# Optimization experiments

Hardware: AMD Instinct MI355X
Metric: run time of the kernel (lower is better)

## Reference

```python
import jax, jax.numpy as jnp
import numpy as np

B, S, HID = 2, 2048, 2048
H, HKV, D = 16, 8, 128
CHUNK = 512
THETA = 1000000.0
NEG = -1e9


def setup_inputs() -> dict:
    key = jax.random.key(0)
    ks = jax.random.split(key, 10)
    hidden_states = jax.random.normal(ks[0], (B, S, HID), dtype=jnp.float32)
    # additive causal mask (0 on/below diagonal, -1e9 above)
    tri = jnp.tril(jnp.ones((S, S), dtype=bool))
    attention_mask = jnp.where(tri, 0.0, NEG).astype(jnp.float32)
    attention_mask = jnp.broadcast_to(attention_mask[None, None], (B, 1, S, S))
    w = 0.02
    Wq = jax.random.normal(ks[1], (HID, H * D), dtype=jnp.float32) * w
    bq = jax.random.normal(ks[2], (H * D,), dtype=jnp.float32) * w
    Wk = jax.random.normal(ks[3], (HID, HKV * D), dtype=jnp.float32) * w
    bk = jax.random.normal(ks[4], (HKV * D,), dtype=jnp.float32) * w
    Wv = jax.random.normal(ks[5], (HID, HKV * D), dtype=jnp.float32) * w
    bv = jax.random.normal(ks[6], (HKV * D,), dtype=jnp.float32) * w
    Wo = jax.random.normal(ks[7], (H * D, HID), dtype=jnp.float32) * w
    bo = jax.random.normal(ks[8], (HID,), dtype=jnp.float32) * w
    return {"hidden_states": hidden_states, "attention_mask": attention_mask,
            "Wq": Wq, "bq": bq, "Wk": Wk, "bk": bk, "Wv": Wv, "bv": bv,
            "Wo": Wo, "bo": bo}


def _rope_tables(seq_len, dim):
    inv_freq = 1.0 / (THETA ** (jnp.arange(0, dim, 2, dtype=jnp.float32) / dim))
    pos = jnp.arange(seq_len, dtype=jnp.float32)
    freqs = pos[:, None] * inv_freq[None, :]          # [S, D/2]
    emb = jnp.concatenate([freqs, freqs], axis=-1)    # [S, D]
    return jnp.cos(emb)[None, None], jnp.sin(emb)[None, None]  # [1,1,S,D]


def _rotate_half(x):
    x1, x2 = jnp.split(x, 2, axis=-1)
    return jnp.concatenate([-x2, x1], axis=-1)


def _attn_forward(hidden_states, attention_mask, Wq, bq, Wk, bk, Wv, bv, Wo, bo):
    bsz, s, _ = hidden_states.shape
    q = (hidden_states @ Wq + bq).reshape(bsz, s, H, D).transpose(0, 2, 1, 3)
    k = (hidden_states @ Wk + bk).reshape(bsz, s, HKV, D).transpose(0, 2, 1, 3)
    v = (hidden_states @ Wv + bv).reshape(bsz, s, HKV, D).transpose(0, 2, 1, 3)
    cos, sin = _rope_tables(s, D)
    q = q * cos + _rotate_half(q) * sin
    k = k * cos + _rotate_half(k) * sin
    n_rep = H // HKV
    k = jnp.repeat(k, n_rep, axis=1)  # repeat_kv
    v = jnp.repeat(v, n_rep, axis=1)
    scale = 1.0 / jnp.sqrt(jnp.float32(D))
    nq, nk = s // CHUNK, s // CHUNK
    Qc = q.reshape(bsz, H, nq, CHUNK, D)
    Kc = jnp.moveaxis(k.reshape(bsz, H, nk, CHUNK, D), 2, 0)   # [nk,B,H,Ck,D]
    Vc = jnp.moveaxis(v.reshape(bsz, H, nk, CHUNK, D), 2, 0)
    Mc = jnp.moveaxis(attention_mask.reshape(bsz, 1, nq, CHUNK, nk, CHUNK), 4, 0)  # [nk,B,1,nq,Cq,Ck]

    def step(carry, xs):
        o, m, d = carry
        k_seg, v_seg, m_seg = xs
        # scores: [B,H,nq,Cq,Ck]
        sc = jnp.einsum('bhqcd,bhkd->bhqck', Qc, k_seg) * scale + m_seg
        new_m = jnp.maximum(m, sc.max(axis=-1, keepdims=True))
        e = jnp.exp(sc - new_m)
        sums = e.sum(axis=-1, keepdims=True)
        prev = jnp.exp(m - new_m)          # NOTE: uses running max, as in source
        d_new = prev + sums
        o = (o * prev + jnp.einsum('bhqck,bhkd->bhqcd', e, v_seg)) / d_new
        return (o, new_m, d_new), None

    o0 = jnp.zeros((bsz, H, nq, CHUNK, D), dtype=jnp.float32)
    m0 = jnp.full((bsz, H, nq, CHUNK, 1), -jnp.inf, dtype=jnp.float32)
    d0 = jnp.ones((bsz, H, nq, CHUNK, 1), dtype=jnp.float32)
    (o, m, d), _ = jax.lax.scan(step, (o0, m0, d0), (Kc, Vc, Mc))
    # final rescale: attn_output * exp(max - logsumexp) == o / d_last (source math)
    o = o / d
    attn = o.reshape(bsz, H, s, D).transpose(0, 2, 1, 3).reshape(bsz, s, H * D)
    return attn @ Wo + bo


def reference(hidden_states, attention_mask, Wq, bq, Wk, bk, Wv, bv, Wo, bo):
    return _attn_forward(hidden_states, attention_mask, Wq, bq, Wk, bk, Wv, bv, Wo, bo)
```

## Files before the change

kernel.cpp:

```cpp
#include <hip/hip_runtime.h>
#include <hip/hip_bf16.h>


typedef __attribute__((ext_vector_type(8))) short s8v;
typedef __attribute__((ext_vector_type(4))) float f4v;

#define MFMA16(a, b, c) __builtin_amdgcn_mfma_f32_16x16x32_bf16((a), (b), (c), 0, 0, 0)

typedef unsigned short u16;
typedef const __attribute__((address_space(1))) unsigned int* gas_p;
typedef __attribute__((address_space(3))) unsigned int* las_p;

__device__ __forceinline__ void gl_lds16(const void* g, void* l) {
    __builtin_amdgcn_global_load_lds((gas_p)g, (las_p)l, 16, 0, 0);
}

__device__ __forceinline__ u16 f2b(float f) {
    __hip_bfloat16 h = __float2bfloat16(f);
    return *reinterpret_cast<u16*>(&h);
}
__device__ __forceinline__ float b2f(u16 u) {
    __hip_bfloat16 h;
    *reinterpret_cast<u16*>(&h) = u;
    return __bfloat162float(h);
}

__device__ const unsigned char qt_tab[40] = {
    4, 5, 6, 7,
    8, 8, 9, 9, 10, 10, 11, 11,
    12, 12, 12, 13, 13, 13, 14, 14, 14, 15, 15, 15,
    3, 7, 11, 15, 2, 6, 10, 14, 1, 5, 9, 13, 0, 4, 8, 12};
__device__ const unsigned char c_tab[40] = {
    0, 0, 0, 0,
    0, 1, 0, 1, 0, 1, 0, 1,
    0, 1, 2, 0, 1, 2, 0, 1, 2, 0, 1, 2,
    0, 1, 2, 3, 0, 1, 2, 3, 0, 1, 2, 3, 0, 1, 2, 3};

__device__ __forceinline__ int uoff40(int qt, int c) {
    int qc = qt >> 2;
    if (c < qc) {
        if (qt < 8) return qt - 4;
        if (qt < 12) return 4 + ((qt - 8) << 1) + c;
        return 12 + (qt - 12) * 3 + c;
    }
    return 24 + ((3 - (qt & 3)) << 2) + qc;
}

__global__ __launch_bounds__(256) void k_cast_hs(const float* __restrict__ src,
                                                 u16* __restrict__ dst) {
    int i = blockIdx.x * 256 + threadIdx.x;
    float4 v = reinterpret_cast<const float4*>(src)[i];
    alignas(8) u16 t[4] = {f2b(v.x), f2b(v.y), f2b(v.z), f2b(v.w)};
    reinterpret_cast<uint2*>(dst)[i] = *reinterpret_cast<uint2*>(t);
}

__global__ __launch_bounds__(256) void k_transpose_w(
    const float* __restrict__ Wq, const float* __restrict__ Wk,
    const float* __restrict__ Wv, const float* __restrict__ Wo,
    u16* __restrict__ wt_all, u16* __restrict__ wo_t) {
    int id = blockIdx.x;
    const float* W; u16* dst; int N, nbase;
    if (id < 4096)      { W = Wq; dst = wt_all; N = 2048; nbase = 0; }
    else if (id < 6144) { W = Wk; dst = wt_all; N = 1024; nbase = 2048; id -= 4096; }
    else if (id < 8192) { W = Wv; dst = wt_all; N = 1024; nbase = 3072; id -= 6144; }
    else                { W = Wo; dst = wo_t;  N = 2048; nbase = 0;    id -= 8192; }
    int tiles_n = N >> 5;
    int k0 = (id / tiles_n) << 5, n0 = (id % tiles_n) << 5;
    __shared__ float t[32][33];
    int tid = threadIdx.x;
    {
        int row = tid >> 3, c4 = (tid & 7) << 2;
        float4 v = *reinterpret_cast<const float4*>(&W[(size_t)(k0 + row) * N + n0 + c4]);
        t[row][c4 + 0] = v.x; t[row][c4 + 1] = v.y;
        t[row][c4 + 2] = v.z; t[row][c4 + 3] = v.w;
    }
    __syncthreads();
    {
        int n = tid >> 3, kq = (tid & 7) << 2;
        alignas(8) u16 p[4];
#pragma unroll
        for (int j = 0; j < 4; j++) p[j] = f2b(t[kq + j][n]);
        *reinterpret_cast<uint2*>(&dst[(size_t)(nbase + n0 + n) * 2048 + k0 + kq]) =
            *reinterpret_cast<uint2*>(p);
    }
}

__global__ __launch_bounds__(256) void k_bias(const float* __restrict__ bq,
                                              const float* __restrict__ bk,
                                              const float* __restrict__ bv,
                                              float* __restrict__ dst) {
    int i = blockIdx.x * 256 + threadIdx.x;
    float v = (i < 2048) ? bq[i] : (i < 3072) ? bk[i - 2048] : bv[i - 3072];
    dst[i] = v;
}

__global__ __launch_bounds__(256) void k_gemm(
    const u16* __restrict__ A, const u16* __restrict__ Bt,
    const float* __restrict__ bias, void* __restrict__ out,
    int M, int N, int K, int out_f32) {
    __shared__ alignas(16) u16 As[128][64];
    __shared__ alignas(16) u16 Bs[128][64];
    int tid = threadIdx.x;
    int wave = tid >> 6, lane = tid & 63, quad = lane >> 4, l16 = lane & 15;
    int m0 = blockIdx.y << 7, n0 = blockIdx.x << 7;
    int wm = (wave >> 1) << 6, wn = (wave & 1) << 6;
    f4v zero = {0.f, 0.f, 0.f, 0.f};
    f4v acc[4][4];
#pragma unroll
    for (int a = 0; a < 4; a++)
#pragma unroll
        for (int b = 0; b < 4; b++) acc[a][b] = zero;
    int r0 = tid >> 3;
    int gsw = (tid & 7) ^ (r0 & 7);
    const u16* gA = A + (size_t)(m0 + r0) * K + (gsw << 3);
    const u16* gB = Bt + (size_t)(n0 + r0) * K + (gsw << 3);
    for (int k0 = 0; k0 < K; k0 += 64) {
        __syncthreads();
#pragma unroll
        for (int i = 0; i < 4; i++) {
            gl_lds16(gA + (size_t)(i << 5) * K + k0, (char*)As + (i << 12) + tid * 16);
            gl_lds16(gB + (size_t)(i << 5) * K + k0, (char*)Bs + (i << 12) + tid * 16);
        }
        __syncthreads();
#pragma unroll
        for (int ks = 0; ks < 2; ks++) {
            int rg = (((ks << 2) | quad) ^ (l16 & 7)) << 3;
            s8v af[4], bf_[4];
#pragma unroll
            for (int mi = 0; mi < 4; mi++)
                af[mi] = *reinterpret_cast<const s8v*>(&As[wm + mi * 16 + l16][rg]);
#pragma unroll
            for (int ni = 0; ni < 4; ni++)
                bf_[ni] = *reinterpret_cast<const s8v*>(&Bs[wn + ni * 16 + l16][rg]);
#pragma unroll
            for (int mi = 0; mi < 4; mi++)
#pragma unroll
                for (int ni = 0; ni < 4; ni++)
                    acc[mi][ni] = MFMA16(af[mi], bf_[ni], acc[mi][ni]);
        }
    }
#pragma unroll
    for (int mi = 0; mi < 4; mi++) {
#pragma unroll
        for (int ni = 0; ni < 4; ni++) {
            int n = n0 + wn + ni * 16 + l16;
            float bsv = bias[n];
#pragma unroll
            for (int r = 0; r < 4; r++) {
                int m = m0 + wm + mi * 16 + (quad << 2) + r;
                float v = acc[mi][ni][r] + bsv;
                if (out_f32)
                    reinterpret_cast<float*>(out)[(size_t)m * N + n] = v;
                else
                    reinterpret_cast<u16*>(out)[(size_t)m * N + n] = f2b(v);
            }
        }
    }
}

__global__ __launch_bounds__(256) void k_rope(const u16* __restrict__ qkv,
                                              u16* __restrict__ qr,
                                              u16* __restrict__ kr) {
    const float qscale = 0.08838834764831845f * 1.44269504088896340f;
    int row = blockIdx.x;
    int b = row >> 11, s = row & 2047;
    const u16* src = qkv + (size_t)row * 4096;
    __shared__ float lcs[64], lsn[64];
    int tid = threadIdx.x;
    if (tid < 64) {
        float fr = (float)s * exp2f((float)tid * -0.31143075889569023f);
        lcs[tid] = cosf(fr);
        lsn[tid] = sinf(fr);
    }
    __syncthreads();
    for (int u = tid; u < 1536; u += 256) {
        int hh, i;
        const u16* sp;
        u16* dp;
        float sc;
        if (u < 1024) {
            hh = u >> 6; i = u & 63;
            sp = src + hh * 128;
            dp = qr + ((size_t)(b * 16 + hh) * 2048 + s) * 128;
            sc = qscale;
        } else {
            int u2 = u - 1024;
            hh = u2 >> 6; i = u2 & 63;
            sp = src + 2048 + hh * 128;
            dp = kr + ((size_t)(b * 8 + hh) * 2048 + s) * 128;
            sc = 1.f;
        }
        float x1 = b2f(sp[i]);
        float x2 = b2f(sp[i + 64]);
        float cs = lcs[i], sn = lsn[i];
        dp[i]      = f2b((x1 * cs - x2 * sn) * sc);
        dp[i + 64] = f2b((x2 * cs + x1 * sn) * sc);
    }
}

__global__ __launch_bounds__(256) void k_vtrans(const u16* __restrict__ qkv,
                                                u16* __restrict__ vt) {
    int bkv = blockIdx.z, b = bkv >> 3, kv = bkv & 7;
    int s0 = blockIdx.x << 6, d0 = blockIdx.y << 5;
    __shared__ alignas(16) u16 t[32][72];
    int tid = threadIdx.x, c = tid & 31, rr = tid >> 5;
#pragma unroll
    for (int i = 0; i < 8; i++) {
        int s = s0 + rr + i * 8;
        t[c][rr + i * 8] = qkv[(size_t)(b * 2048 + s) * 4096 + 3072 + kv * 128 + d0 + c];
    }
    __syncthreads();
    int dd = tid >> 3, sc8 = (tid & 7) << 3;
    *reinterpret_cast<uint4*>(&vt[((size_t)(b * 8 + kv) * 128 + d0 + dd) * 2048 + s0 + sc8]) =
        *reinterpret_cast<const uint4*>(&t[dd][sc8]);
}

__global__ __launch_bounds__(256) void k_attn_part(const u16* __restrict__ qr,
                                                   const u16* __restrict__ kr,
                                                   const u16* __restrict__ vt,
                                                   u16* __restrict__ PVp,
                                                   float* __restrict__ scp) {
    const float NINF = -__builtin_inff();
    __shared__ alignas(16) u16 Ks[2][64 * 128];
    __shared__ alignas(16) u16 Vs[2][128 * 64];
    __shared__ alignas(16) u16 Pb[4][2][16][40];

    int tid = threadIdx.x;
    int wv = tid >> 6, lane = tid & 63, quad = lane >> 4, l16 = lane & 15;
    int x = blockIdx.x, h = blockIdx.y, b = blockIdx.z, kvh = h >> 1;
    int qt = qt_tab[x], c = c_tab[x], qc = qt >> 2;
    bool diag = (c == qc);
    int m3 = qt & 3;
    int nt = diag ? ((m3 + 1) << 1) : 8;
    int kbase = c << 9;
    const u16* Qp = qr + ((size_t)(b * 16 + h) * 2048 + qt * 128 + wv * 32) * 128;
    const u16* Kp = kr + ((size_t)(b * 8 + kvh) * 2048) * 128;
    const u16* Vp = vt + ((size_t)(b * 8 + kvh) * 128) * 2048;

    s8v qf0[4], qf1[4];
#pragma unroll
    for (int sl = 0; sl < 4; sl++) {
        qf0[sl] = *reinterpret_cast<const s8v*>(&Qp[l16 * 128 + sl * 32 + (quad << 3)]);
        qf1[sl] = *reinterpret_cast<const s8v*>(&Qp[(16 + l16) * 128 + sl * 32 + (quad << 3)]);
    }
    s8v ones;
#pragma unroll
    for (int i = 0; i < 8; i++) ones[i] = (short)0x3F80;

    int krow = tid >> 4, kg = (tid & 15) ^ krow;
    int vd = tid >> 3, vg = (tid & 7) ^ (vd & 7);
    auto stage = [&](int t) {
        int kbt = kbase + (t << 6);
        const u16* kgp = Kp + (size_t)(kbt + krow) * 128 + (kg << 3);
        const u16* vgp = Vp + (size_t)vd * 2048 + kbt + (vg << 3);
        char* kd = (char*)&Ks[t & 1][0];
        char* vdst = (char*)&Vs[t & 1][0];
#pragma unroll
        for (int i = 0; i < 4; i++) {
            gl_lds16(kgp + (size_t)(i << 4) * 128, kd + (i << 12) + tid * 16);
            gl_lds16(vgp + (size_t)(i << 5) * 2048, vdst + (i << 12) + tid * 16);
        }
    };

    f4v zero = {0.f, 0.f, 0.f, 0.f};
    f4v u0[8], u1[8], sums0 = zero, sums1 = zero;
#pragma unroll
    for (int ni = 0; ni < 8; ni++) { u0[ni] = zero; u1[ni] = zero; }
    float tmx0[4] = {NINF, NINF, NINF, NINF};
    float tmx1[4] = {NINF, NINF, NINF, NINF};
    int qg0 = wv << 1, qg1 = (wv << 1) + 1;

    stage(0);
    for (int t = 0; t < nt; t++) {
        __syncthreads();
        if (t + 1 < nt) stage(t + 1);
        const char* Kbuf = (const char*)&Ks[t & 1][0];
        const char* Vbuf = (const char*)&Vs[t & 1][0];
        int kgb = diag ? ((t << 2) - (m3 << 3)) : -1000;

#pragma unroll
        for (int s2 = 0; s2 < 2; s2++) {
            if (kgb + (s2 << 1) > qg1) continue;
            bool h0act = (kgb + (s2 << 1) <= qg0);
#pragma unroll
            for (int half = 0; half < 2; half++) {
                int sub = (s2 << 1) + half;
                int kgi = kgb + sub;
                if (kgi > qg1) {
                    if (h0act)
#pragma unroll
                        for (int r = 0; r < 4; r++)
                            Pb[wv][0][(quad << 2) + r][(half << 4) + l16] = (u16)0;
#pragma unroll
                    for (int r = 0; r < 4; r++)
                        Pb[wv][1][(quad << 2) + r][(half << 4) + l16] = (u16)0;
                    continue;
                }
                bool act0 = (kgi <= qg0);
                f4v s0 = zero, s1 = zero;
#pragma unroll
                for (int sl = 0; sl < 4; sl++) {
                    s8v kf = *reinterpret_cast<const s8v*>(
                        Kbuf + ((sub << 4) + l16) * 256 + ((((sl << 2) + quad) ^ l16) << 4));
                    if (act0) s0 = MFMA16(qf0[sl], kf, s0);
                    s1 = MFMA16(qf1[sl], kf, s1);
                }
                if (act0) {
                    bool tri = (kgi == qg0);
#pragma unroll
                    for (int r = 0; r < 4; r++) {
                        float v = s0[r];
                        if (tri && (l16 > (quad << 2) + r)) v = NINF;
                        tmx0[r] = fmaxf(tmx0[r], v);
                        Pb[wv][0][(quad << 2) + r][(half << 4) + l16] =
                            f2b(__builtin_amdgcn_exp2f(v));
                    }
                } else if (h0act) {
#pragma unroll
                    for (int r = 0; r < 4; r++)
                        Pb[wv][0][(quad << 2) + r][(half << 4) + l16] = (u16)0;
                }
                {
                    bool tri = (kgi == qg1);
#pragma unroll
                    for (int r = 0; r < 4; r++) {
                        float v = s1[r];
                        if (tri && (l16 > (quad << 2) + r)) v = NINF;
                        tmx1[r] = fmaxf(tmx1[r], v);
                        Pb[wv][1][(quad << 2) + r][(half << 4) + l16] =
                            f2b(__builtin_amdgcn_exp2f(v));
                    }
                }
            }
            s8v pf0, pf1;
            if (h0act) {
                pf0 = *reinterpret_cast<const s8v*>(&Pb[wv][0][l16][quad << 3]);
                sums0 = MFMA16(pf0, ones, sums0);
            }
            pf1 = *reinterpret_cast<const s8v*>(&Pb[wv][1][l16][quad << 3]);
            sums1 = MFMA16(pf1, ones, sums1);
#pragma unroll
            for (int ni = 0; ni < 8; ni++) {
                s8v vf = *reinterpret_cast<const s8v*>(
                    Vbuf + ((ni << 4) + l16) * 128 + ((((s2 << 2) + quad) ^ (l16 & 7)) << 4));
                if (h0act) u0[ni] = MFMA16(pf0, vf, u0[ni]);
                u1[ni] = MFMA16(pf1, vf, u1[ni]);
            }
        }
    }
#pragma unroll
    for (int r = 0; r < 4; r++) {
#pragma unroll
        for (int off = 1; off < 16; off <<= 1) {
            tmx0[r] = fmaxf(tmx0[r], __shfl_xor(tmx0[r], off));
            tmx1[r] = fmaxf(tmx1[r], __shfl_xor(tmx1[r], off));
        }
    }
    float resc0[4], resc1[4];
#pragma unroll
    for (int r = 0; r < 4; r++) {
        resc0[r] = __builtin_amdgcn_exp2f(-tmx0[r]);
        resc1[r] = __builtin_amdgcn_exp2f(-tmx1[r]);
    }
    int slot = (b * 16 + h) * 40 + x;
    u16* pvdst = PVp + (size_t)slot * 16384;
    int row0 = wv * 32 + (quad << 2);
#pragma unroll
    for (int ni = 0; ni < 8; ni++)
#pragma unroll
        for (int r = 0; r < 4; r++) {
            pvdst[(row0 + r) * 128 + ni * 16 + l16] = f2b(u0[ni][r] * resc0[r]);
            pvdst[(row0 + 16 + r) * 128 + ni * 16 + l16] = f2b(u1[ni][r] * resc1[r]);
        }
    if (l16 == 0) {
        float* scd = scp + (size_t)slot * 256 + row0;
#pragma unroll
        for (int r = 0; r < 4; r++) {
            scd[r] = tmx0[r] * 0.6931471805599453f;
            scd[16 + r] = tmx1[r] * 0.6931471805599453f;
            scd[128 + r] = sums0[r] * resc0[r];
            scd[144 + r] = sums1[r] * resc1[r];
        }
    }
}

__global__ __launch_bounds__(256) void k_attn_comb(const u16* __restrict__ PVp,
                                                   const float* __restrict__ scp,
                                                   u16* __restrict__ attnb) {
    int qt64 = blockIdx.x, h = blockIdx.y, b = blockIdx.z;
    int qt = qt64 >> 1, qc = qt >> 2;
    int tid = threadIdx.x;
    int row = ((qt64 & 1) << 6) + (tid >> 2), d0 = (tid & 3) << 5;
    int bh = b * 16 + h;
    float o[32];
#pragma unroll
    for (int i = 0; i < 32; i++) o[i] = 0.f;
    float mprev = -__builtin_inff(), dlast = 1.f;
    for (int cc = 0; cc <= qc; cc++) {
        int slot = bh * 40 + uoff40(qt, cc);
        float ch = scp[(size_t)slot * 256 + row];
        float sh = scp[(size_t)slot * 256 + 128 + row];
        float mnew = fmaxf(mprev, ch);
        float p = __expf(mprev - mnew);
        float lam = __expf(ch - mnew);
        float dd = p + lam * sh;
        float inv = 1.f / dd;
        const u16* pv = PVp + (size_t)slot * 16384 + row * 128 + d0;
#pragma unroll
        for (int k = 0; k < 4; k++) {
            s8v v8 = *reinterpret_cast<const s8v*>(pv + (k << 3));
#pragma unroll
            for (int j = 0; j < 8; j++) {
                int i = (k << 3) + j;
                o[i] = (o[i] * p + lam * b2f((u16)v8[j])) * inv;
            }
        }
        mprev = mnew;
        dlast = dd;
    }
    if (qc == 3) {
        float inv = 1.f / dlast;
#pragma unroll
        for (int i = 0; i < 32; i++) o[i] *= inv;
    }
    alignas(16) u16 ob[32];
#pragma unroll
    for (int i = 0; i < 32; i++) ob[i] = f2b(o[i]);
    u16* dst = attnb + (size_t)(b * 2048 + qt * 128 + row) * 2048 + h * 128 + d0;
#pragma unroll
    for (int k = 0; k < 4; k++)
        reinterpret_cast<uint4*>(dst)[k] = reinterpret_cast<const uint4*>(ob)[k];
}

extern "C" void kernel_launch(void* const* d_in, const int* in_sizes, int n_in,
                              void* d_out, int out_size, void* d_ws, size_t ws_size,
                              hipStream_t stream) {
    (void)in_sizes; (void)n_in; (void)out_size; (void)ws_size;
    const float* hs = (const float*)d_in[0];
    const float* Wq = (const float*)d_in[2];
    const float* bq = (const float*)d_in[3];
    const float* Wk = (const float*)d_in[4];
    const float* bk = (const float*)d_in[5];
    const float* Wv = (const float*)d_in[6];
    const float* bv = (const float*)d_in[7];
    const float* Wo = (const float*)d_in[8];
    const float* bo = (const float*)d_in[9];

    char* ws = (char*)d_ws;
    u16* hsb      = (u16*)(ws);
    u16* qr       = hsb;
    u16* attnb    = hsb;
    u16* wt_all   = (u16*)(ws + (16u << 20));
    u16* kr       = wt_all;
    u16* vt       = (u16*)(ws + (24u << 20));
    u16* wo_t     = (u16*)(ws + (32u << 20));
    float* bias_c = (float*)(ws + (40u << 20));
    u16* qkv      = (u16*)(ws + (40u << 20) + 65536);
    u16* PVp      = qkv;
    float* scp    = (float*)(ws + (40u << 20) + 65536 + 41943040u);

    k_cast_hs<<<8192, 256, 0, stream>>>(hs, hsb);
    k_transpose_w<<<12288, 256, 0, stream>>>(Wq, Wk, Wv, Wo, wt_all, wo_t);
    k_bias<<<16, 256, 0, stream>>>(bq, bk, bv, bias_c);
    k_gemm<<<dim3(32, 32), 256, 0, stream>>>(hsb, wt_all, bias_c, qkv,
                                             4096, 4096, 2048, 0);
    k_rope<<<4096, 256, 0, stream>>>(qkv, qr, kr);
    k_vtrans<<<dim3(32, 4, 16), 256, 0, stream>>>(qkv, vt);
    k_attn_part<<<dim3(40, 16, 2), 256, 0, stream>>>(qr, kr, vt, PVp, scp);
    k_attn_comb<<<dim3(32, 16, 2), 256, 0, stream>>>(PVp, scp, attnb);
    k_gemm<<<dim3(16, 32), 256, 0, stream>>>(attnb, wo_t, bo, d_out,
                                             4096, 2048, 2048, 1);
}
```

Measured before the change: 425.3 us.

## Keep softmax probabilities in registers via transposed QK MFMA and permlane swaps

Computes S^T by swapping the MFMA operand order, so each lane holds one query row's scores. The scores are then packed to bf16 and rearranged across lanes with permlane32/16 swaps to form the A operand of the PV MFMA directly. This removes the per-wave LDS staging buffer for P, along with its writes and reads. The row max becomes a per-lane scalar reduced over two shuffle steps instead of four, then broadcast back per row. The risks are the correctness of the lane permutation and the builtin/asm availability on gfx950.

```diff
diff --git a/kernel.cpp b/kernel.cpp
--- a/kernel.cpp
+++ b/kernel.cpp
@@ -4,6 +4,7 @@
 
 typedef __attribute__((ext_vector_type(8))) short s8v;
 typedef __attribute__((ext_vector_type(4))) float f4v;
+typedef __attribute__((ext_vector_type(4))) unsigned int u32x4;
 
 #define MFMA16(a, b, c) __builtin_amdgcn_mfma_f32_16x16x32_bf16((a), (b), (c), 0, 0, 0)
 
@@ -23,6 +24,21 @@
     __hip_bfloat16 h;
     *reinterpret_cast<u16*>(&h) = u;
     return __bfloat162float(h);
+}
+
+__device__ __forceinline__ void qswap(unsigned int& a, unsigned int& b) {
+#if __has_builtin(__builtin_amdgcn_permlane32_swap) && __has_builtin(__builtin_amdgcn_permlane16_swap)
+    typedef __attribute__((ext_vector_type(2))) unsigned int u32x2;
+    u32x2 r1 = __builtin_amdgcn_permlane32_swap(a, b, false, false);
+    u32x2 r2 = __builtin_amdgcn_permlane16_swap(r1[0], r1[1], false, false);
+    a = r2[0]; b = r2[1];
+#else
+    asm volatile("v_permlane32_swap_b32 %0, %1\n\t"
+                 "s_nop 0\n\t"
+                 "v_permlane16_swap_b32 %0, %1\n\t"
+                 "s_nop 0"
+                 : "+v"(a), "+v"(b));
+#endif
 }
 
 __device__ const unsigned char qt_tab[40] = {
@@ -223,7 +239,6 @@
     const float NINF = -__builtin_inff();
     __shared__ alignas(16) u16 Ks[2][64 * 128];
     __shared__ alignas(16) u16 Vs[2][128 * 64];
-    __shared__ alignas(16) u16 Pb[4][2][16][40];
 
     int tid = threadIdx.x;
     int wv = tid >> 6, lane = tid & 63, quad = lane >> 4, l16 = lane & 15;
@@ -262,12 +277,26 @@
         }
     };
 
+    auto pack = [&](const f4v& s, bool tri, bool act, float& tmx,
+                    unsigned int& wlo, unsigned int& whi) {
+        if (!act) { wlo = 0u; whi = 0u; return; }
+        float e[4];
+#pragma unroll
+        for (int r = 0; r < 4; r++) {
+            float v = s[r];
+            if (tri && ((quad << 2) + r > l16)) v = NINF;
+            tmx = fmaxf(tmx, v);
+            e[r] = __builtin_amdgcn_exp2f(v);
+        }
+        wlo = (unsigned int)f2b(e[0]) | ((unsigned int)f2b(e[1]) << 16);
+        whi = (unsigned int)f2b(e[2]) | ((unsigned int)f2b(e[3]) << 16);
+    };
+
     f4v zero = {0.f, 0.f, 0.f, 0.f};
     f4v u0[8], u1[8], sums0 = zero, sums1 = zero;
 #pragma unroll
     for (int ni = 0; ni < 8; ni++) { u0[ni] = zero; u1[ni] = zero; }
-    float tmx0[4] = {NINF, NINF, NINF, NINF};
-    float tmx1[4] = {NINF, NINF, NINF, NINF};
+    float tmx0 = NINF, tmx1 = NINF;
     int qg0 = wv << 1, qg1 = (wv << 1) + 1;
 
     stage(0);
@@ -280,87 +309,67 @@
 
 #pragma unroll
         for (int s2 = 0; s2 < 2; s2++) {
-            if (kgb + (s2 << 1) > qg1) continue;
-            bool h0act = (kgb + (s2 << 1) <= qg0);
-#pragma unroll
-            for (int half = 0; half < 2; half++) {
-                int sub = (s2 << 1) + half;
-                int kgi = kgb + sub;
-                if (kgi > qg1) {
-                    if (h0act)
-#pragma unroll
-                        for (int r = 0; r < 4; r++)
-                            Pb[wv][0][(quad << 2) + r][(half << 4) + l16] = (u16)0;
-#pragma unroll
-                    for (int r = 0; r < 4; r++)
-                        Pb[wv][1][(quad << 2) + r][(half << 4) + l16] = (u16)0;
-                    continue;
-                }
-                bool act0 = (kgi <= qg0);
-                f4v s0 = zero, s1 = zero;
+            int kgA = kgb + (s2 << 1);
+            if (kgA > qg1) continue;
+            int kgB = kgA + 1;
+            bool a0 = (kgA <= qg0), b0 = (kgB <= qg0), b1 = (kgB <= qg1);
+            f4v sA0 = zero, sA1 = zero, sB0 = zero, sB1 = zero;
+#pragma unroll
+            for (int sl = 0; sl < 4; sl++) {
+                s8v kf = *reinterpret_cast<const s8v*>(
+                    Kbuf + (((s2 << 1) << 4) + l16) * 256 +
+                    ((((sl << 2) + quad) ^ l16) << 4));
+                if (a0) sA0 = MFMA16(kf, qf0[sl], sA0);
+                sA1 = MFMA16(kf, qf1[sl], sA1);
+            }
+            if (b1) {
 #pragma unroll
                 for (int sl = 0; sl < 4; sl++) {
                     s8v kf = *reinterpret_cast<const s8v*>(
-                        Kbuf + ((sub << 4) + l16) * 256 + ((((sl << 2) + quad) ^ l16) << 4));
-                    if (act0) s0 = MFMA16(qf0[sl], kf, s0);
-                    s1 = MFMA16(qf1[sl], kf, s1);
+                        Kbuf + ((((s2 << 1) | 1) << 4) + l16) * 256 +
+                        ((((sl << 2) + quad) ^ l16) << 4));
+                    if (b0) sB0 = MFMA16(kf, qf0[sl], sB0);
+                    sB1 = MFMA16(kf, qf1[sl], sB1);
                 }
-                if (act0) {
-                    bool tri = (kgi == qg0);
-#pragma unroll
-                    for (int r = 0; r < 4; r++) {
-                        float v = s0[r];
-                        if (tri && (l16 > (quad << 2) + r)) v = NINF;
-                        tmx0[r] = fmaxf(tmx0[r], v);
-                        Pb[wv][0][(quad << 2) + r][(half << 4) + l16] =
-                            f2b(__builtin_amdgcn_exp2f(v));
-                    }
-                } else if (h0act) {
-#pragma unroll
-                    for (int r = 0; r < 4; r++)
-                        Pb[wv][0][(quad << 2) + r][(half << 4) + l16] = (u16)0;
-                }
-                {
-                    bool tri = (kgi == qg1);
-#pragma unroll
-                    for (int r = 0; r < 4; r++) {
-                        float v = s1[r];
-                        if (tri && (l16 > (quad << 2) + r)) v = NINF;
-                        tmx1[r] = fmaxf(tmx1[r], v);
-                        Pb[wv][1][(quad << 2) + r][(half << 4) + l16] =
-                            f2b(__builtin_amdgcn_exp2f(v));
-                    }
-                }
-            }
-            s8v pf0, pf1;
-            if (h0act) {
-                pf0 = *reinterpret_cast<const s8v*>(&Pb[wv][0][l16][quad << 3]);
-                sums0 = MFMA16(pf0, ones, sums0);
-            }
-            pf1 = *reinterpret_cast<const s8v*>(&Pb[wv][1][l16][quad << 3]);
-            sums1 = MFMA16(pf1, ones, sums1);
+            }
+            unsigned int A0w, A1w, B0w, B1w;
+            pack(sA1, kgA == qg1, true, tmx1, A0w, A1w);
+            pack(sB1, kgB == qg1, b1, tmx1, B0w, B1w);
+            qswap(A0w, B0w); qswap(A1w, B1w);
+            u32x4 pw1 = {A0w, A1w, B0w, B1w};
+            s8v pa1 = __builtin_bit_cast(s8v, pw1);
+            sums1 = MFMA16(pa1, ones, sums1);
+            s8v pa0 = pa1;
+            if (a0) {
+                unsigned int C0w, C1w, D0w, D1w;
+                pack(sA0, kgA == qg0, true, tmx0, C0w, C1w);
+                pack(sB0, kgB == qg0, b0, tmx0, D0w, D1w);
+                qswap(C0w, D0w); qswap(C1w, D1w);
+                u32x4 pw0 = {C0w, C1w, D0w, D1w};
+                pa0 = __builtin_bit_cast(s8v, pw0);
+                sums0 = MFMA16(pa0, ones, sums0);
+            }
 #pragma unroll
             for (int ni = 0; ni < 8; ni++) {
                 s8v vf = *reinterpret_cast<const s8v*>(
-                    Vbuf + ((ni << 4) + l16) * 128 + ((((s2 << 2) + quad) ^ (l16 & 7)) << 4));
-                if (h0act) u0[ni] = MFMA16(pf0, vf, u0[ni]);
-                u1[ni] = MFMA16(pf1, vf, u1[ni]);
-            }
-        }
-    }
+                    Vbuf + ((ni << 4) + l16) * 128 +
+                    ((((s2 << 2) + quad) ^ (l16 & 7)) << 4));
+                if (a0) u0[ni] = MFMA16(pa0, vf, u0[ni]);
+                u1[ni] = MFMA16(pa1, vf, u1[ni]);
+            }
+        }
+    }
+    tmx0 = fmaxf(tmx0, __shfl_xor(tmx0, 16));
+    tmx0 = fmaxf(tmx0, __shfl_xor(tmx0, 32));
+    tmx1 = fmaxf(tmx1, __shfl_xor(tmx1, 16));
+    tmx1 = fmaxf(tmx1, __shfl_xor(tmx1, 32));
+    float m0[4], m1[4], resc0[4], resc1[4];
 #pragma unroll
     for (int r = 0; r < 4; r++) {
-#pragma unroll
-        for (int off = 1; off < 16; off <<= 1) {
-            tmx0[r] = fmaxf(tmx0[r], __shfl_xor(tmx0[r], off));
-            tmx1[r] = fmaxf(tmx1[r], __shfl_xor(tmx1[r], off));
-        }
-    }
-    float resc0[4], resc1[4];
-#pragma unroll
-    for (int r = 0; r < 4; r++) {
-        resc0[r] = __builtin_amdgcn_exp2f(-tmx0[r]);
-        resc1[r] = __builtin_amdgcn_exp2f(-tmx1[r]);
+        m0[r] = __shfl(tmx0, (quad << 2) + r);
+        m1[r] = __shfl(tmx1, (quad << 2) + r);
+        resc0[r] = __builtin_amdgcn_exp2f(-m0[r]);
+        resc1[r] = __builtin_amdgcn_exp2f(-m1[r]);
     }
     int slot = (b * 16 + h) * 40 + x;
     u16* pvdst = PVp + (size_t)slot * 16384;
@@ -376,8 +385,8 @@
         float* scd = scp + (size_t)slot * 256 + row0;
 #pragma unroll
         for (int r = 0; r < 4; r++) {
-            scd[r] = tmx0[r] * 0.6931471805599453f;
-            scd[16 + r] = tmx1[r] * 0.6931471805599453f;
+            scd[r] = m0[r] * 0.6931471805599453f;
+            scd[16 + r] = m1[r] * 0.6931471805599453f;
             scd[128 + r] = sums0[r] * resc0[r];
             scd[144 + r] = sums1[r] * resc1[r];
         }
```

Result: no change. 417.4 us (-1.9%).
